# Optimization experiments

Measured on AMD Instinct MI355X. Metric: run time of the kernel, lower is better.

Reference implementation:

```python
import jax, jax.numpy as jnp
import numpy as np

N = 65536    # collocation points
N1 = 1024    # RBF centers
EPS = 0.1    # multiscale parameter used for width init scale


def setup_inputs() -> dict:
    key = jax.random.key(0)
    ks = jax.random.split(key, 10)
    x = jax.random.uniform(ks[0], (N, 2), dtype=jnp.float32)

    def mk(i):
        h = jax.random.uniform(ks[3 * i + 1], (N1,), dtype=jnp.float32)
        c = jax.random.uniform(ks[3 * i + 2], (N1, 2), dtype=jnp.float32)
        w = 5.0 * jax.random.uniform(ks[3 * i + 3], (N1, 2), dtype=jnp.float32) / EPS
        return h, c, w

    h1, c1, w1 = mk(0)
    h2, c2, w2 = mk(1)
    h3, c3, w3 = mk(2)
    return dict(x=x, hight=h1, center=c1, width=w1,
                hight2=h2, center2=c2, width2=w2,
                hight3=h3, center3=c3, width3=w3)


def _rbf(X, c, h, w):
    """Gaussian RBF expansion. X:(N,2) points, c:(N1,2) centers,
    h:(N1,) heights, w:(N1,2) widths. Returns u, du/dx, du/dy, each (N,)."""
    x1 = X[:, 0:1] - c[None, :, 0]          # (N, N1)
    y1 = X[:, 1:2] - c[None, :, 1]          # (N, N1)
    d1 = w[:, 0] ** 2                        # (N1,)
    d2 = w[:, 1] ** 2                        # (N1,)
    e = jnp.exp(-(x1 ** 2) * d1 - (y1 ** 2) * d2)  # (N, N1)
    u = e @ h                                # (N,)
    ux = (-2.0 * x1 * d1 * e) @ h            # (N,)
    uy = (-2.0 * y1 * d2 * e) @ h            # (N,)
    return u, ux, uy


def reference(x, hight, center, width, hight2, center2, width2,
              hight3, center3, width3):
    _, ux, uy = _rbf(x, center, hight, width)
    P, Px, _ = _rbf(x, center2, hight2, width2)
    Q, _, Qy = _rbf(x, center3, hight3, width3)
    return (ux, uy, P, Px, Q, Qy)
```

## Files before the change

### kernel.cpp

```cpp
#include <hip/hip_runtime.h>
#include <math.h>

#define N_PTS 65536
#define N_CTR 1024
#define CHUNK 256
#define PPB   512

#if __has_builtin(__builtin_amdgcn_exp2f)
#define EXP2(x) __builtin_amdgcn_exp2f(x)
#else
#define EXP2(x) exp2f(x)
#endif

__global__ __launch_bounds__(256) void srbf_kernel(
    const float* __restrict__ x,
    const float* __restrict__ h0, const float* __restrict__ c0, const float* __restrict__ w0,
    const float* __restrict__ h1, const float* __restrict__ c1, const float* __restrict__ w1,
    const float* __restrict__ h2, const float* __restrict__ c2, const float* __restrict__ w2,
    float* __restrict__ out)
{
    __shared__ float4 sA[CHUNK];
    __shared__ float4 sB[CHUNK];
    __shared__ float  sC[CHUNK];

    const int bid   = blockIdx.x;
    const int set   = bid >> 9;
    const int r     = bid & 511;
    const int chunk = r >> 7;
    const int pblk  = r & 127;
    const int tid   = threadIdx.x;

    const float*  __restrict__ h = (set == 0) ? h0 : ((set == 1) ? h1 : h2);
    const float2* __restrict__ c = (const float2*)((set == 0) ? c0 : ((set == 1) ? c1 : c2));
    const float2* __restrict__ w = (const float2*)((set == 0) ? w0 : ((set == 1) ? w1 : w2));

    const float LOG2E = 1.4426950408889634f;

    {
        const int j = chunk * CHUNK + tid;
        float2 cj = c[j];
        float2 wj = w[j];
        float  hh = h[j];
        float d1 = wj.x * wj.x;
        float d2 = wj.y * wj.y;
        float zb =  2.f * cj.x * d1 * LOG2E;
        float zc = -d1 * LOG2E;
        float zd =  2.f * cj.y * d2 * LOG2E;
        float ze = -d2 * LOG2E;
        float za = -(cj.x * cj.x * d1 + cj.y * cj.y * d2) * LOG2E;
        float k0, k1, k2, k3;
        if (set == 0) {
            k0 = -2.f * hh * d1;
            k1 =  2.f * hh * d1 * cj.x;
            k2 = -2.f * hh * d2;
            k3 =  2.f * hh * d2 * cj.y;
        } else if (set == 1) {
            k0 = hh;
            k1 = -2.f * hh * d1;
            k2 =  2.f * hh * d1 * cj.x;
            k3 = 0.f;
        } else {
            k0 = hh;
            k1 = -2.f * hh * d2;
            k2 =  2.f * hh * d2 * cj.y;
            k3 = 0.f;
        }
        sA[tid] = make_float4(zb, zc, zd, ze);
        sB[tid] = make_float4(za, k0, k1, k2);
        sC[tid] = k3;
    }
    __syncthreads();

    const int i0 = pblk * PPB + tid;
    const int i1 = i0 + 256;
    const float2 Pa = ((const float2*)x)[i0];
    const float2 Pb = ((const float2*)x)[i1];
    const float xa = Pa.x, ya = Pa.y, xb = Pb.x, yb = Pb.y;
    const float xa2 = xa * xa, ya2 = ya * ya, xb2 = xb * xb, yb2 = yb * yb;

    if (set == 0) {
        float aP0 = 0.f, aQ0 = 0.f, aP1 = 0.f, aQ1 = 0.f;
        float bP0 = 0.f, bQ0 = 0.f, bP1 = 0.f, bQ1 = 0.f;
        #pragma unroll 4
        for (int jj = 0; jj < CHUNK; ++jj) {
            float4 A = sA[jj];
            float4 B = sB[jj];
            float  k3 = sC[jj];
            float sa = fmaf(xa, A.x, B.x);
            sa = fmaf(xa2, A.y, sa);
            sa = fmaf(ya,  A.z, sa);
            sa = fmaf(ya2, A.w, sa);
            float sb = fmaf(xb, A.x, B.x);
            sb = fmaf(xb2, A.y, sb);
            sb = fmaf(yb,  A.z, sb);
            sb = fmaf(yb2, A.w, sb);
            float ea = EXP2(sa);
            float eb = EXP2(sb);
            aP0 = fmaf(B.y, ea, aP0);  aQ0 = fmaf(B.z, ea, aQ0);
            aP1 = fmaf(B.w, ea, aP1);  aQ1 = fmaf(k3,  ea, aQ1);
            bP0 = fmaf(B.y, eb, bP0);  bQ0 = fmaf(B.z, eb, bQ0);
            bP1 = fmaf(B.w, eb, bP1);  bQ1 = fmaf(k3,  eb, bQ1);
        }
        atomicAdd(&out[i0],          fmaf(xa, aP0, aQ0));
        atomicAdd(&out[N_PTS + i0],  fmaf(ya, aP1, aQ1));
        atomicAdd(&out[i1],          fmaf(xb, bP0, bQ0));
        atomicAdd(&out[N_PTS + i1],  fmaf(yb, bP1, bQ1));
    } else {
        float aU = 0.f, aP = 0.f, aQ = 0.f;
        float bU = 0.f, bP = 0.f, bQ = 0.f;
        #pragma unroll 4
        for (int jj = 0; jj < CHUNK; ++jj) {
            float4 A = sA[jj];
            float4 B = sB[jj];
            float sa = fmaf(xa, A.x, B.x);
            sa = fmaf(xa2, A.y, sa);
            sa = fmaf(ya,  A.z, sa);
            sa = fmaf(ya2, A.w, sa);
            float sb = fmaf(xb, A.x, B.x);
            sb = fmaf(xb2, A.y, sb);
            sb = fmaf(yb,  A.z, sb);
            sb = fmaf(yb2, A.w, sb);
            float ea = EXP2(sa);
            float eb = EXP2(sb);
            aU = fmaf(B.y, ea, aU);
            aP = fmaf(B.z, ea, aP);
            aQ = fmaf(B.w, ea, aQ);
            bU = fmaf(B.y, eb, bU);
            bP = fmaf(B.z, eb, bP);
            bQ = fmaf(B.w, eb, bQ);
        }
        float* o = out + (size_t)set * 2 * N_PTS;
        const float ga = (set == 1) ? xa : ya;
        const float gb = (set == 1) ? xb : yb;
        atomicAdd(&o[i0],         aU);
        atomicAdd(&o[N_PTS + i0], fmaf(ga, aP, aQ));
        atomicAdd(&o[i1],         bU);
        atomicAdd(&o[N_PTS + i1], fmaf(gb, bP, bQ));
    }
}

extern "C" void kernel_launch(void* const* d_in, const int* in_sizes, int n_in,
                              void* d_out, int out_size, void* d_ws, size_t ws_size,
                              hipStream_t stream) {
    const float* x  = (const float*)d_in[0];
    const float* h1 = (const float*)d_in[1];
    const float* c1 = (const float*)d_in[2];
    const float* w1 = (const float*)d_in[3];
    const float* h2 = (const float*)d_in[4];
    const float* c2 = (const float*)d_in[5];
    const float* w2 = (const float*)d_in[6];
    const float* h3 = (const float*)d_in[7];
    const float* c3 = (const float*)d_in[8];
    const float* w3 = (const float*)d_in[9];

    hipMemsetAsync(d_out, 0, (size_t)out_size * sizeof(float), stream);

    srbf_kernel<<<dim3(3 * 4 * 128), dim3(256), 0, stream>>>(
        x, h1, c1, w1, h2, c2, w2, h3, c3, w3, (float*)d_out);
}
```

Measured before the change: 62.51 us.

## Process eight points per thread with smaller center chunks for register reuse

Each thread now evaluates 8 collocation points per center instead of 2, with 128-center chunks and 2048 points per block. This amortizes the shared-memory reads of center coefficients over more points and increases instruction-level parallelism. In exchange, the grid shrinks to 768 blocks, register pressure rises, and the number of atomic partial-sum writes doubles because there are more center chunks.

```diff
diff --git a/kernel.cpp b/kernel.cpp
--- a/kernel.cpp
+++ b/kernel.cpp
@@ -1,10 +1,11 @@
 #include <hip/hip_runtime.h>
 #include <math.h>
 
-#define N_PTS 65536
-#define N_CTR 1024
-#define CHUNK 256
-#define PPB   512
+#define N_PTS  65536
+#define N_CTR  1024
+#define CHUNK  128
+#define PPT    8
+#define PPB    (256 * PPT)
 
 #if __has_builtin(__builtin_amdgcn_exp2f)
 #define EXP2(x) __builtin_amdgcn_exp2f(x)
@@ -24,10 +25,10 @@
     __shared__ float  sC[CHUNK];
 
     const int bid   = blockIdx.x;
-    const int set   = bid >> 9;
-    const int r     = bid & 511;
-    const int chunk = r >> 7;
-    const int pblk  = r & 127;
+    const int set   = bid >> 8;
+    const int r     = bid & 255;
+    const int chunk = r >> 5;
+    const int pblk  = r & 31;
     const int tid   = threadIdx.x;
 
     const float*  __restrict__ h = (set == 0) ? h0 : ((set == 1) ? h1 : h2);
@@ -36,7 +37,7 @@
 
     const float LOG2E = 1.4426950408889634f;
 
-    {
+    if (tid < CHUNK) {
         const int j = chunk * CHUNK + tid;
         float2 cj = c[j];
         float2 wj = w[j];
@@ -71,71 +72,74 @@
     }
     __syncthreads();
 
-    const int i0 = pblk * PPB + tid;
-    const int i1 = i0 + 256;
-    const float2 Pa = ((const float2*)x)[i0];
-    const float2 Pb = ((const float2*)x)[i1];
-    const float xa = Pa.x, ya = Pa.y, xb = Pb.x, yb = Pb.y;
-    const float xa2 = xa * xa, ya2 = ya * ya, xb2 = xb * xb, yb2 = yb * yb;
+    const int base = pblk * PPB + tid;
+
+    float X[PPT], Y[PPT], X2[PPT], Y2[PPT];
+    #pragma unroll
+    for (int p = 0; p < PPT; ++p) {
+        float2 q = ((const float2*)x)[base + p * 256];
+        X[p] = q.x;  Y[p] = q.y;
+        X2[p] = q.x * q.x;  Y2[p] = q.y * q.y;
+    }
 
     if (set == 0) {
-        float aP0 = 0.f, aQ0 = 0.f, aP1 = 0.f, aQ1 = 0.f;
-        float bP0 = 0.f, bQ0 = 0.f, bP1 = 0.f, bQ1 = 0.f;
-        #pragma unroll 4
-        for (int jj = 0; jj < CHUNK; ++jj) {
-            float4 A = sA[jj];
-            float4 B = sB[jj];
-            float  k3 = sC[jj];
-            float sa = fmaf(xa, A.x, B.x);
-            sa = fmaf(xa2, A.y, sa);
-            sa = fmaf(ya,  A.z, sa);
-            sa = fmaf(ya2, A.w, sa);
-            float sb = fmaf(xb, A.x, B.x);
-            sb = fmaf(xb2, A.y, sb);
-            sb = fmaf(yb,  A.z, sb);
-            sb = fmaf(yb2, A.w, sb);
-            float ea = EXP2(sa);
-            float eb = EXP2(sb);
-            aP0 = fmaf(B.y, ea, aP0);  aQ0 = fmaf(B.z, ea, aQ0);
-            aP1 = fmaf(B.w, ea, aP1);  aQ1 = fmaf(k3,  ea, aQ1);
-            bP0 = fmaf(B.y, eb, bP0);  bQ0 = fmaf(B.z, eb, bQ0);
-            bP1 = fmaf(B.w, eb, bP1);  bQ1 = fmaf(k3,  eb, bQ1);
+        float A0[PPT], A1[PPT], A2[PPT], A3[PPT];
+        #pragma unroll
+        for (int p = 0; p < PPT; ++p) { A0[p] = A1[p] = A2[p] = A3[p] = 0.f; }
+
+        #pragma unroll 2
+        for (int j = 0; j < CHUNK; ++j) {
+            float4 A = sA[j];
+            float4 B = sB[j];
+            float  k3 = sC[j];
+            #pragma unroll
+            for (int p = 0; p < PPT; ++p) {
+                float s = fmaf(X[p],  A.x, B.x);
+                s       = fmaf(X2[p], A.y, s);
+                s       = fmaf(Y[p],  A.z, s);
+                s       = fmaf(Y2[p], A.w, s);
+                float e = EXP2(s);
+                A0[p] = fmaf(B.y, e, A0[p]);
+                A1[p] = fmaf(B.z, e, A1[p]);
+                A2[p] = fmaf(B.w, e, A2[p]);
+                A3[p] = fmaf(k3,  e, A3[p]);
+            }
         }
-        atomicAdd(&out[i0],          fmaf(xa, aP0, aQ0));
-        atomicAdd(&out[N_PTS + i0],  fmaf(ya, aP1, aQ1));
-        atomicAdd(&out[i1],          fmaf(xb, bP0, bQ0));
-        atomicAdd(&out[N_PTS + i1],  fmaf(yb, bP1, bQ1));
+        #pragma unroll
+        for (int p = 0; p < PPT; ++p) {
+            const int i = base + p * 256;
+            atomicAdd(&out[i],         fmaf(X[p], A0[p], A1[p]));
+            atomicAdd(&out[N_PTS + i], fmaf(Y[p], A2[p], A3[p]));
+        }
     } else {
-        float aU = 0.f, aP = 0.f, aQ = 0.f;
-        float bU = 0.f, bP = 0.f, bQ = 0.f;
-        #pragma unroll 4
-        for (int jj = 0; jj < CHUNK; ++jj) {
-            float4 A = sA[jj];
-            float4 B = sB[jj];
-            float sa = fmaf(xa, A.x, B.x);
-            sa = fmaf(xa2, A.y, sa);
-            sa = fmaf(ya,  A.z, sa);
-            sa = fmaf(ya2, A.w, sa);
-            float sb = fmaf(xb, A.x, B.x);
-            sb = fmaf(xb2, A.y, sb);
-            sb = fmaf(yb,  A.z, sb);
-            sb = fmaf(yb2, A.w, sb);
-            float ea = EXP2(sa);
-            float eb = EXP2(sb);
-            aU = fmaf(B.y, ea, aU);
-            aP = fmaf(B.z, ea, aP);
-            aQ = fmaf(B.w, ea, aQ);
-            bU = fmaf(B.y, eb, bU);
-            bP = fmaf(B.z, eb, bP);
-            bQ = fmaf(B.w, eb, bQ);
+        float A0[PPT], A1[PPT], A2[PPT];
+        #pragma unroll
+        for (int p = 0; p < PPT; ++p) { A0[p] = A1[p] = A2[p] = 0.f; }
+
+        #pragma unroll 2
+        for (int j = 0; j < CHUNK; ++j) {
+            float4 A = sA[j];
+            float4 B = sB[j];
+            #pragma unroll
+            for (int p = 0; p < PPT; ++p) {
+                float s = fmaf(X[p],  A.x, B.x);
+                s       = fmaf(X2[p], A.y, s);
+                s       = fmaf(Y[p],  A.z, s);
+                s       = fmaf(Y2[p], A.w, s);
+                float e = EXP2(s);
+                A0[p] = fmaf(B.y, e, A0[p]);
+                A1[p] = fmaf(B.z, e, A1[p]);
+                A2[p] = fmaf(B.w, e, A2[p]);
+            }
         }
         float* o = out + (size_t)set * 2 * N_PTS;
-        const float ga = (set == 1) ? xa : ya;
-        const float gb = (set == 1) ? xb : yb;
-        atomicAdd(&o[i0],         aU);
-        atomicAdd(&o[N_PTS + i0], fmaf(ga, aP, aQ));
-        atomicAdd(&o[i1],         bU);
-        atomicAdd(&o[N_PTS + i1], fmaf(gb, bP, bQ));
+        #pragma unroll
+        for (int p = 0; p < PPT; ++p) {
+            const int i = base + p * 256;
+            const float g = (set == 1) ? X[p] : Y[p];
+            atomicAdd(&o[i],         A0[p]);
+            atomicAdd(&o[N_PTS + i], fmaf(g, A1[p], A2[p]));
+        }
     }
 }
 
@@ -155,6 +159,6 @@
 
     hipMemsetAsync(d_out, 0, (size_t)out_size * sizeof(float), stream);
 
-    srbf_kernel<<<dim3(3 * 4 * 128), dim3(256), 0, stream>>>(
+    srbf_kernel<<<dim3(768), dim3(256), 0, stream>>>(
         x, h1, c1, w1, h2, c2, w2, h3, c3, w3, (float*)d_out);
 }
```

Result: faster. 55.21 us (-11.7%).
